# Performance work log

Hardware: AMD Instinct MI355X
Metric: run time of the kernel (lower is better)

## Reference

```python
import jax, jax.numpy as jnp
import numpy as np

N_NODES = 4096
D_FEAT = 256


def _interp_linear_2x(x):
    # Matches F.interpolate(mode='linear', scale_factor=2, align_corners=False)
    # applied along the node axis. x: [N, D] -> [2N, D]
    n = x.shape[0]
    out_i = jnp.arange(2 * n, dtype=jnp.float32)
    src = jnp.clip((out_i + 0.5) * 0.5 - 0.5, 0.0, float(n - 1))
    i0 = jnp.floor(src).astype(jnp.int32)
    i1 = jnp.minimum(i0 + 1, n - 1)
    w = (src - i0.astype(jnp.float32))[:, None]
    return x[i0] * (1.0 - w) + x[i1] * w


def _nearest_neighbor_idx(x):
    # argmin over pairwise Euclidean distances with diagonal excluded.
    # Squared distances give the same argmin as torch.cdist.
    sq = jnp.sum(x * x, axis=1)
    d2 = sq[:, None] + sq[None, :] - 2.0 * (x @ x.T)  # [2N, 2N]
    m = x.shape[0]
    d2 = jnp.where(jnp.eye(m, dtype=bool), jnp.inf, d2)
    return jnp.argmin(d2, axis=1)


def setup_inputs() -> dict:
    key = jax.random.key(0)
    k1, k2, k3, k4 = jax.random.split(key, 4)
    x = jax.random.normal(k1, (N_NODES, D_FEAT), dtype=jnp.float32)
    adj = jax.random.uniform(k2, (N_NODES, N_NODES), dtype=jnp.float32)
    # Xavier-uniform-ish init for the two GCN weights
    lim = float(np.sqrt(6.0 / (D_FEAT + D_FEAT)))
    W1 = jax.random.uniform(k3, (D_FEAT, D_FEAT), jnp.float32, -lim, lim)
    W2 = jax.random.uniform(k4, (D_FEAT, D_FEAT), jnp.float32, -lim, lim)
    return {"x": x, "adj": adj, "W1": W1, "W2": W2}


def reference(x, adj, W1, W2):
    # conv1: adj @ (x @ W1)
    h = adj @ (x @ W1)                      # [N, D]
    x2 = _interp_linear_2x(h)               # [2N, D]
    # nearest-neighbor one-hot adjacency, then conv2.
    # one_hot(nn_idx) @ support == support[nn_idx] (exact same math)
    nn_idx = _nearest_neighbor_idx(x2)      # [2N]
    support = x2 @ W2                       # [2N, D]
    return support[nn_idx]                  # [2N, D]
```

## Files before the change

kernel.cpp:

```cpp
#include <hip/hip_runtime.h>
#include <hip/hip_bf16.h>
#include <cstdint>

typedef __attribute__((ext_vector_type(8))) __bf16 bf16x8;
typedef __attribute__((ext_vector_type(4))) float f32x4;

static __device__ __forceinline__ unsigned short f2bf(float f) {
  return __builtin_bit_cast(unsigned short, (__bf16)f);
}
static __device__ __forceinline__ unsigned pack2(float a, float b) {
  return (unsigned)f2bf(a) | ((unsigned)f2bf(b) << 16);
}
#define GLDS(src, dst) __builtin_amdgcn_global_load_lds( \
    (const __attribute__((address_space(1))) void*)(src), \
    (__attribute__((address_space(3))) void*)(dst), 16, 0, 0)


__global__ void transpose_w_kernel(const float* __restrict__ W1, const float* __restrict__ W2,
                                   unsigned short* __restrict__ W1t, unsigned short* __restrict__ W2t) {
  int i = blockIdx.x * 256 + threadIdx.x;
  int k = i >> 8, n = i & 255;
  W1t[n * 256 + k] = f2bf(W1[k * 256 + n]);
  W2t[n * 256 + k] = f2bf(W2[k * 256 + n]);
}

__global__ void upsample_kernel(const unsigned short* __restrict__ hs,
                                unsigned short* __restrict__ x2b, float* __restrict__ sq) {
  int row = blockIdx.x * 4 + (threadIdx.x >> 6);
  int c = (threadIdx.x & 63) * 4;
  float s = (row + 0.5f) * 0.5f - 0.5f;
  s = fminf(fmaxf(s, 0.0f), 4095.0f);
  float fl = floorf(s);
  int i0 = (int)fl;
  int i1 = min((int)fl + 1, 4095);
  float w = s - fl;
  float v0[4] = {0.f, 0.f, 0.f, 0.f}, v1[4] = {0.f, 0.f, 0.f, 0.f};
  #pragma unroll
  for (int k = 0; k < 8; ++k) {
    ushort4 u0 = *(const ushort4*)&hs[(size_t)k * 4096 * 256 + i0 * 256 + c];
    ushort4 u1 = *(const ushort4*)&hs[(size_t)k * 4096 * 256 + i1 * 256 + c];
    v0[0] += __builtin_bit_cast(float, (unsigned)u0.x << 16);
    v0[1] += __builtin_bit_cast(float, (unsigned)u0.y << 16);
    v0[2] += __builtin_bit_cast(float, (unsigned)u0.z << 16);
    v0[3] += __builtin_bit_cast(float, (unsigned)u0.w << 16);
    v1[0] += __builtin_bit_cast(float, (unsigned)u1.x << 16);
    v1[1] += __builtin_bit_cast(float, (unsigned)u1.y << 16);
    v1[2] += __builtin_bit_cast(float, (unsigned)u1.z << 16);
    v1[3] += __builtin_bit_cast(float, (unsigned)u1.w << 16);
  }
  float p = 0.f;
  ushort4 st;
  unsigned short* sp = (unsigned short*)&st;
  #pragma unroll
  for (int e = 0; e < 4; ++e) {
    float v = v0[e] * (1.0f - w) + v1[e] * w;
    sp[e] = f2bf(v);
    p += v * v;
  }
  *(ushort4*)&x2b[(size_t)row * 256 + c] = st;
  #pragma unroll
  for (int m = 32; m > 0; m >>= 1) p += __shfl_down(p, m, 64);
  if ((threadIdx.x & 63) == 0) sq[row] = p;
}

__launch_bounds__(512)
__global__ void adj_gemm_kernel(const float* __restrict__ adjp,
                                const unsigned short* __restrict__ Ttp,
                                unsigned short* __restrict__ hs) {
  constexpr int NT = 8;
  __shared__ alignas(16) unsigned short As[256 * 64];
  __shared__ alignas(16) unsigned short Bs[256 * 64];

  const int tid = threadIdx.x;
  const int wid = tid >> 6;
  const int lane = tid & 63;
  const int g = lane >> 4, lr = lane & 15;
  const int wr = wid >> 2;
  const int wc = wid & 3;
  const int m0 = blockIdx.x * 256;
  const int kbase = blockIdx.y * 512;
  unsigned short* outp = hs + (size_t)blockIdx.y * 4096 * 256;

  const int srow = tid >> 3;
  const int scp = tid & 7;
  const int ssc = scp ^ (srow & 7);
  const float* aB[4];
  const unsigned short* bB[4];
  #pragma unroll
  for (int it = 0; it < 4; ++it) {
    aB[it] = adjp + (size_t)(m0 + it * 64 + srow) * 4096 + kbase + ssc * 8;
    bB[it] = Ttp + (size_t)(it * 64 + srow) * 4096 + kbase + ssc * 8;
  }

  f32x4 acc[8][4];
  const f32x4 fzero = {0.f, 0.f, 0.f, 0.f};
  #pragma unroll
  for (int i = 0; i < 8; ++i)
    #pragma unroll
    for (int j = 0; j < 4; ++j) acc[i][j] = fzero;

  #pragma unroll
  for (int t = 0; t < NT; ++t) {
    #pragma unroll
    for (int it = 0; it < 4; ++it)
      GLDS(bB[it] + t * 64, Bs + (size_t)(it * 512 + wid * 64) * 8);
    #pragma unroll
    for (int it = 0; it < 4; ++it) {
      const float* src = aB[it] + t * 64;
      float4 f0 = *(const float4*)src;
      float4 f1 = *(const float4*)(src + 4);
      uint4 pk = { pack2(f0.x, f0.y), pack2(f0.z, f0.w),
                   pack2(f1.x, f1.y), pack2(f1.z, f1.w) };
      *(uint4*)&As[(it * 64 + srow) * 64 + scp * 8] = pk;
    }
    __syncthreads();
    #pragma unroll
    for (int kk = 0; kk < 2; ++kk) {
      const int ch = (kk * 4 + g) ^ (lr & 7);
      bf16x8 b[4];
      #pragma unroll
      for (int j = 0; j < 4; ++j)
        b[j] = *(const bf16x8*)&Bs[(wc * 64 + j * 16 + lr) * 64 + ch * 8];
      #pragma unroll
      for (int i = 0; i < 8; ++i) {
        bf16x8 a = *(const bf16x8*)&As[(wr * 128 + i * 16 + lr) * 64 + ch * 8];
        #pragma unroll
        for (int j = 0; j < 4; ++j)
          acc[i][j] = __builtin_amdgcn_mfma_f32_16x16x32_bf16(a, b[j], acc[i][j], 0, 0, 0);
      }
    }
    __syncthreads();
  }

  #pragma unroll
  for (int i = 0; i < 8; ++i) {
    int mrow = m0 + wr * 128 + i * 16 + g * 4;
    #pragma unroll
    for (int j = 0; j < 4; ++j) {
      int col = wc * 64 + j * 16 + lr;
      #pragma unroll
      for (int r = 0; r < 4; ++r)
        outp[(size_t)(mrow + r) * 256 + col] = f2bf(acc[i][j][r]);
    }
  }
}

__launch_bounds__(256, 3)
__global__ void gram_kernel(const unsigned short* __restrict__ X,
                            const float* __restrict__ sq,
                            unsigned* __restrict__ pv) {
  __shared__ alignas(16) unsigned short As[128 * 64];
  __shared__ alignas(16) unsigned short Bs[128 * 64];
  __shared__ unsigned mrgr[2][128];
  __shared__ unsigned mrgc[2][128];

  const int tid = threadIdx.x;
  const int wid = tid >> 6;
  const int lane = tid & 63;
  const int g = lane >> 4, lr = lane & 15;
  const int wr = wid >> 1, wc = wid & 1;

  int t0 = blockIdx.x;
  int t = (t0 & 7) * 260 + (t0 >> 3);
  int bi = (int)((sqrtf(8.0f * (float)t + 1.0f) - 1.0f) * 0.5f);
  while ((bi + 1) * (bi + 2) / 2 <= t) ++bi;
  while (bi * (bi + 1) / 2 > t) --bi;
  const int bx = bi;
  const int by = t - bi * (bi + 1) / 2;
  const int m0 = bx * 128;
  const int n0 = by * 128;
  const bool diag = (bx == by);

  const int srow = tid >> 3;
  const int ssc = (tid & 7) ^ (srow & 7);
  const unsigned short* aBase = X + (size_t)(m0 + srow) * 256 + ssc * 8;
  const unsigned short* bBase = X + (size_t)(n0 + srow) * 256 + ssc * 8;
  unsigned short* const aDst = As + (size_t)(tid >> 6) * 512;
  unsigned short* const bDst = Bs + (size_t)(tid >> 6) * 512;
  const unsigned short* const Bsrc = diag ? As : Bs;

  f32x4 acc[4][4];
  const f32x4 fzero = {0.f, 0.f, 0.f, 0.f};
  #pragma unroll
  for (int i = 0; i < 4; ++i)
    #pragma unroll
    for (int j = 0; j < 4; ++j) acc[i][j] = fzero;

  #pragma unroll
  for (int ks = 0; ks < 4; ++ks) {
    #pragma unroll
    for (int it = 0; it < 4; ++it)
      GLDS(aBase + it * 8192 + ks * 64, aDst + it * 2048);
    if (!diag) {
      #pragma unroll
      for (int it = 0; it < 4; ++it)
        GLDS(bBase + it * 8192 + ks * 64, bDst + it * 2048);
    }
    __syncthreads();
    #pragma unroll
    for (int kk = 0; kk < 2; ++kk) {
      const int ch = (kk * 4 + g) ^ (lr & 7);
      bf16x8 b[4];
      #pragma unroll
      for (int j = 0; j < 4; ++j)
        b[j] = *(const bf16x8*)&Bsrc[(wc * 64 + j * 16 + lr) * 64 + ch * 8];
      #pragma unroll
      for (int i = 0; i < 4; ++i) {
        bf16x8 a = *(const bf16x8*)&As[(wr * 64 + i * 16 + lr) * 64 + ch * 8];
        #pragma unroll
        for (int j = 0; j < 4; ++j)
          acc[i][j] = __builtin_amdgcn_mfma_f32_16x16x32_bf16(a, b[j], acc[i][j], 0, 0, 0);
      }
    }
    __syncthreads();
  }

  int jcol[4];
  float sqj[4];
  unsigned ckey[4];
  #pragma unroll
  for (int j = 0; j < 4; ++j) {
    jcol[j] = n0 + wc * 64 + j * 16 + lr;
    sqj[j] = sq[jcol[j]];
    ckey[j] = 0xFFFFFFFFu;
  }
  #pragma unroll
  for (int i = 0; i < 4; ++i) {
    #pragma unroll
    for (int r = 0; r < 4; ++r) {
      const int lrow = wr * 64 + i * 16 + g * 4 + r;
      const int irow = m0 + lrow;
      const float sqi = sq[irow];
      unsigned rk = 0xFFFFFFFFu;
      #pragma unroll
      for (int j = 0; j < 4; ++j) {
        float v = fmaf(-2.0f, acc[i][j][r], sqi + sqj[j]);
        unsigned bits = __float_as_uint(v) & 0xFFFFE000u;
        unsigned krow = bits | (unsigned)jcol[j];
        if (diag && jcol[j] == irow) krow = 0xFFFFFFFFu;
        rk = min(rk, krow);
        if (!diag) ckey[j] = min(ckey[j], bits | (unsigned)irow);
      }
      #pragma unroll
      for (int m = 1; m < 16; m <<= 1)
        rk = min(rk, (unsigned)__shfl_xor((int)rk, m, 64));
      if (lr == 0) mrgr[wc][lrow] = rk;
    }
  }
  if (!diag) {
    #pragma unroll
    for (int j = 0; j < 4; ++j) {
      ckey[j] = min(ckey[j], (unsigned)__shfl_xor((int)ckey[j], 16, 64));
      ckey[j] = min(ckey[j], (unsigned)__shfl_xor((int)ckey[j], 32, 64));
      if (g == 0) mrgc[wr][wc * 64 + j * 16 + lr] = ckey[j];
    }
  }
  __syncthreads();
  if (tid < 128) {
    pv[(size_t)by * 8192 + m0 + tid] = min(mrgr[0][tid], mrgr[1][tid]);
  } else if (!diag) {
    int c = tid - 128;
    pv[(size_t)(64 + bx) * 8192 + n0 + c] = min(mrgc[0][c], mrgc[1][c]);
  }
}

template <int BM, int BN, int WAVES_M, int KT, int EPI, bool AF32, bool GATHER>
__launch_bounds__(256)
__global__ void gemm_nt_kernel(const void* __restrict__ Ap, int lda,
                               const unsigned short* __restrict__ Bp, int ldb,
                               int M, int N,
                               float* __restrict__ Cf,
                               unsigned short* __restrict__ Cb,
                               const unsigned* __restrict__ pv) {
  constexpr int BK = 64;
  constexpr int NT = KT / BK;
  constexpr int WAVES_N = 4 / WAVES_M;
  constexpr int WM = BM / WAVES_M;
  constexpr int WN = BN / WAVES_N;
  constexpr int FM = WM / 16;
  constexpr int FN = WN / 16;
  constexpr int ASLOT = BM * 8;
  constexpr int AITER = (ASLOT + 255) / 256;
  constexpr int BITER = (BN * 8) / 256;

  __shared__ alignas(16) unsigned short As[BM * BK];
  __shared__ alignas(16) unsigned short Bs[BN * BK];
  __shared__ unsigned redp[GATHER ? 4 * 64 : 1];
  __shared__ unsigned pckl[GATHER ? 64 : 1];

  const int tid = threadIdx.x;
  const int wid = tid >> 6;
  const int lane = tid & 63;
  const int g = lane >> 4;
  const int lr = lane & 15;
  const int wr = wid / WAVES_N;
  const int wc = wid % WAVES_N;
  const int m0 = blockIdx.x * BM;
  const int n0 = blockIdx.y * BN;

  if constexpr (GATHER) {
    static_assert(!GATHER || BM == 64, "inline reduce assumes BM==64");
    const int row = tid & 63;
    const int part = tid >> 6;
    const int cr = m0 >> 7;
    unsigned best = 0xFFFFFFFFu;
    #pragma unroll
    for (int s8 = 0; s8 < 16; ++s8) {
      int s = part * 16 + s8;
      int slot = s + (s > cr ? 64 : 0);
      best = min(best, pv[(size_t)slot * 8192 + m0 + row]);
    }
    redp[part * 64 + row] = best;
    __syncthreads();
    if (tid < 64)
      pckl[tid] = min(min(redp[tid], redp[64 + tid]),
                      min(redp[128 + tid], redp[192 + tid])) & 0x1FFFu;
    __syncthreads();
  }

  const int srow = tid >> 3;
  const int ssc = (tid & 7) ^ (srow & 7);
  const float* aBF[AITER];
  const unsigned short* aBH[AITER];
  #pragma unroll
  for (int it = 0; it < AITER; ++it) {
    int r = m0 + srow + it * 32;
    if constexpr (AF32) {
      aBF[it] = (const float*)Ap + (size_t)r * (size_t)lda + ssc * 8;
    } else {
      int sr = GATHER ? (int)pckl[srow + it * 32] : r;
      aBH[it] = (const unsigned short*)Ap + (size_t)sr * (size_t)lda + ssc * 8;
    }
  }
  const unsigned short* bBase = Bp + (size_t)(n0 + srow) * (size_t)ldb + ssc * 8;
  unsigned short* const sDst = As + (size_t)wid * 512;
  unsigned short* const bDst = Bs + (size_t)wid * 512;

  f32x4 acc[FM][FN];
  const f32x4 fzero = {0.f, 0.f, 0.f, 0.f};
  #pragma unroll
  for (int i = 0; i < FM; ++i)
    #pragma unroll
    for (int j = 0; j < FN; ++j) acc[i][j] = fzero;

  #pragma unroll
  for (int t = 0; t < NT; ++t) {
    #pragma unroll
    for (int it = 0; it < BITER; ++it)
      GLDS(bBase + (size_t)it * 32 * ldb + t * 64, bDst + it * 2048);
    if constexpr (AF32) {
      #pragma unroll
      for (int it = 0; it < AITER; ++it) {
        if (ASLOT % 256 == 0 || it * 256 + tid < ASLOT) {
          const float* src = aBF[it] + t * 64;
          float4 f0 = *(const float4*)src;
          float4 f1 = *(const float4*)(src + 4);
          uint4 pk = { pack2(f0.x, f0.y), pack2(f0.z, f0.w),
                       pack2(f1.x, f1.y), pack2(f1.z, f1.w) };
          *(uint4*)&As[(it * 32 + srow) * BK + (tid & 7) * 8] = pk;
        }
      }
    } else {
      #pragma unroll
      for (int it = 0; it < AITER; ++it)
        GLDS(aBH[it] + t * 64, sDst + it * 2048);
    }
    __syncthreads();
    #pragma unroll
    for (int kk = 0; kk < 2; ++kk) {
      const int ch = (kk * 4 + g) ^ (lr & 7);
      bf16x8 a[FM], b[FN];
      #pragma unroll
      for (int i = 0; i < FM; ++i)
        a[i] = *(const bf16x8*)&As[(wr * WM + i * 16 + lr) * BK + ch * 8];
      #pragma unroll
      for (int j = 0; j < FN; ++j)
        b[j] = *(const bf16x8*)&Bs[(wc * WN + j * 16 + lr) * BK + ch * 8];
      #pragma unroll
      for (int i = 0; i < FM; ++i)
        #pragma unroll
        for (int j = 0; j < FN; ++j)
          acc[i][j] = __builtin_amdgcn_mfma_f32_16x16x32_bf16(a[i], b[j], acc[i][j], 0, 0, 0);
    }
    __syncthreads();
  }

  const int rowb = wr * WM;
  const int colb = wc * WN;
  if constexpr (EPI == 0) {
    #pragma unroll
    for (int i = 0; i < FM; ++i) {
      int mrow = m0 + rowb + i * 16 + g * 4;
      #pragma unroll
      for (int j = 0; j < FN; ++j) {
        int col = n0 + colb + j * 16 + lr;
        #pragma unroll
        for (int r = 0; r < 4; ++r)
          Cf[(size_t)(mrow + r) * N + col] = acc[i][j][r];
      }
    }
  } else {
    #pragma unroll
    for (int i = 0; i < FM; ++i) {
      int mrow = m0 + rowb + i * 16 + g * 4;
      #pragma unroll
      for (int j = 0; j < FN; ++j) {
        int col = n0 + colb + j * 16 + lr;
        ushort4 st;
        st.x = f2bf(acc[i][j][0]);
        st.y = f2bf(acc[i][j][1]);
        st.z = f2bf(acc[i][j][2]);
        st.w = f2bf(acc[i][j][3]);
        *(ushort4*)&Cb[(size_t)col * M + mrow] = st;
      }
    }
  }
}


extern "C" void kernel_launch(void* const* d_in, const int* in_sizes, int n_in,
                              void* d_out, int out_size, void* d_ws, size_t ws_size,
                              hipStream_t stream) {
  (void)in_sizes; (void)n_in; (void)out_size; (void)ws_size;
  const float* x   = (const float*)d_in[0];
  const float* adj = (const float*)d_in[1];
  const float* W1  = (const float*)d_in[2];
  const float* W2  = (const float*)d_in[3];
  float* out = (float*)d_out;

  char* p = (char*)d_ws;
  unsigned short* Tt  = (unsigned short*)p;  p += 4096 * 256 * 2;
  char* R             = p;                   p += 16 * 1024 * 1024;
  unsigned short* x2b = (unsigned short*)p;  p += 8192 * 256 * 2;
  float* sqv          = (float*)p;           p += 8192 * 4;
  unsigned short* W1t = (unsigned short*)p;  p += 256 * 256 * 2;
  unsigned short* W2t = (unsigned short*)p;  p += 256 * 256 * 2;

  unsigned short* hs = (unsigned short*)R;
  unsigned* pv       = (unsigned*)R;

  transpose_w_kernel<<<256, 256, 0, stream>>>(W1, W2, W1t, W2t);

  gemm_nt_kernel<64, 64, 4, 256, 1, true, false><<<dim3(64, 4), 256, 0, stream>>>(
      x, 256, W1t, 256, 4096, 256, nullptr, Tt, nullptr);

  adj_gemm_kernel<<<dim3(16, 8), 512, 0, stream>>>(adj, Tt, hs);

  upsample_kernel<<<2048, 256, 0, stream>>>(hs, x2b, sqv);

  gram_kernel<<<2080, 256, 0, stream>>>(x2b, sqv, pv);

  gemm_nt_kernel<64, 64, 4, 256, 0, false, true><<<dim3(128, 4), 256, 0, stream>>>(
      x2b, 256, W2t, 256, 8192, 256, out, nullptr, pv);
}
```

Baseline: 98.81 us.

## Load adj fp32 tiles asynchronously into LDS and convert to bf16 at fragment read

The adjacency GEMM now stages fp32 adj tiles straight into shared memory with global_load_lds and converts them to bf16 only when building MFMA fragments, so the synchronous register round-trip for the A operand goes away. The block tile shrinks from 256x256 with 512 threads to 64x256 with 256 threads, giving 512 blocks instead of 128 for better CU coverage, at the cost of reloading the B tile more often. The gram kernel also drops its blockIdx swizzle and uses a linear triangular tile order instead.

```diff
diff --git a/kernel.cpp b/kernel.cpp
--- a/kernel.cpp
+++ b/kernel.cpp
@@ -63,67 +63,70 @@
   if ((threadIdx.x & 63) == 0) sq[row] = p;
 }
 
-__launch_bounds__(512)
+__launch_bounds__(256)
 __global__ void adj_gemm_kernel(const float* __restrict__ adjp,
                                 const unsigned short* __restrict__ Ttp,
                                 unsigned short* __restrict__ hs) {
   constexpr int NT = 8;
-  __shared__ alignas(16) unsigned short As[256 * 64];
+  __shared__ alignas(16) float Asf[64 * 64];
   __shared__ alignas(16) unsigned short Bs[256 * 64];
 
   const int tid = threadIdx.x;
   const int wid = tid >> 6;
   const int lane = tid & 63;
   const int g = lane >> 4, lr = lane & 15;
-  const int wr = wid >> 2;
-  const int wc = wid & 3;
-  const int m0 = blockIdx.x * 256;
+  const int m0 = blockIdx.x * 64;
   const int kbase = blockIdx.y * 512;
   unsigned short* outp = hs + (size_t)blockIdx.y * 4096 * 256;
 
-  const int srow = tid >> 3;
-  const int scp = tid & 7;
-  const int ssc = scp ^ (srow & 7);
+  const int arow = tid >> 4;
+  const int acp = tid & 15;
+  const int asc = acp ^ (arow & 7);
   const float* aB[4];
-  const unsigned short* bB[4];
-  #pragma unroll
-  for (int it = 0; it < 4; ++it) {
-    aB[it] = adjp + (size_t)(m0 + it * 64 + srow) * 4096 + kbase + ssc * 8;
-    bB[it] = Ttp + (size_t)(it * 64 + srow) * 4096 + kbase + ssc * 8;
-  }
-
-  f32x4 acc[8][4];
+  #pragma unroll
+  for (int it = 0; it < 4; ++it)
+    aB[it] = adjp + (size_t)(m0 + it * 16 + arow) * 4096 + kbase + asc * 4;
+  float* const aDst = Asf + (size_t)wid * 256;
+
+  const int brow = tid >> 3;
+  const int bsc = (tid & 7) ^ (brow & 7);
+  const unsigned short* bBase = Ttp + (size_t)brow * 4096 + kbase + bsc * 8;
+  unsigned short* const bDst = Bs + (size_t)wid * 512;
+
+  f32x4 acc[4][4];
   const f32x4 fzero = {0.f, 0.f, 0.f, 0.f};
   #pragma unroll
-  for (int i = 0; i < 8; ++i)
+  for (int i = 0; i < 4; ++i)
     #pragma unroll
     for (int j = 0; j < 4; ++j) acc[i][j] = fzero;
 
+  const float4* Asf4 = (const float4*)Asf;
+
   #pragma unroll
   for (int t = 0; t < NT; ++t) {
     #pragma unroll
+    for (int it = 0; it < 8; ++it)
+      GLDS(bBase + (size_t)it * 32 * 4096 + t * 64, bDst + it * 2048);
+    #pragma unroll
     for (int it = 0; it < 4; ++it)
-      GLDS(bB[it] + t * 64, Bs + (size_t)(it * 512 + wid * 64) * 8);
-    #pragma unroll
-    for (int it = 0; it < 4; ++it) {
-      const float* src = aB[it] + t * 64;
-      float4 f0 = *(const float4*)src;
-      float4 f1 = *(const float4*)(src + 4);
-      uint4 pk = { pack2(f0.x, f0.y), pack2(f0.z, f0.w),
-                   pack2(f1.x, f1.y), pack2(f1.z, f1.w) };
-      *(uint4*)&As[(it * 64 + srow) * 64 + scp * 8] = pk;
-    }
+      GLDS(aB[it] + t * 64, aDst + it * 1024);
     __syncthreads();
     #pragma unroll
     for (int kk = 0; kk < 2; ++kk) {
-      const int ch = (kk * 4 + g) ^ (lr & 7);
+      const int chb = (kk * 4 + g) ^ (lr & 7);
       bf16x8 b[4];
       #pragma unroll
       for (int j = 0; j < 4; ++j)
-        b[j] = *(const bf16x8*)&Bs[(wc * 64 + j * 16 + lr) * 64 + ch * 8];
-      #pragma unroll
-      for (int i = 0; i < 8; ++i) {
-        bf16x8 a = *(const bf16x8*)&As[(wr * 128 + i * 16 + lr) * 64 + ch * 8];
+        b[j] = *(const bf16x8*)&Bs[(wid * 64 + j * 16 + lr) * 64 + chb * 8];
+      const int c0 = kk * 8 + g * 2;
+      #pragma unroll
+      for (int i = 0; i < 4; ++i) {
+        const int row = i * 16 + lr;
+        float4 f0 = Asf4[row * 16 + (c0 ^ (lr & 7))];
+        float4 f1 = Asf4[row * 16 + ((c0 + 1) ^ (lr & 7))];
+        uint4 pk = { pack2(f0.x, f0.y), pack2(f0.z, f0.w),
+                     pack2(f1.x, f1.y), pack2(f1.z, f1.w) };
+        bf16x8 a = __builtin_bit_cast(bf16x8, pk);
         #pragma unroll
         for (int j = 0; j < 4; ++j)
           acc[i][j] = __builtin_amdgcn_mfma_f32_16x16x32_bf16(a, b[j], acc[i][j], 0, 0, 0);
@@ -133,11 +136,11 @@
   }
 
   #pragma unroll
-  for (int i = 0; i < 8; ++i) {
-    int mrow = m0 + wr * 128 + i * 16 + g * 4;
+  for (int i = 0; i < 4; ++i) {
+    int mrow = m0 + i * 16 + g * 4;
     #pragma unroll
     for (int j = 0; j < 4; ++j) {
-      int col = wc * 64 + j * 16 + lr;
+      int col = wid * 64 + j * 16 + lr;
       #pragma unroll
       for (int r = 0; r < 4; ++r)
         outp[(size_t)(mrow + r) * 256 + col] = f2bf(acc[i][j][r]);
@@ -160,8 +163,7 @@
   const int g = lane >> 4, lr = lane & 15;
   const int wr = wid >> 1, wc = wid & 1;
 
-  int t0 = blockIdx.x;
-  int t = (t0 & 7) * 260 + (t0 >> 3);
+  int t = blockIdx.x;
   int bi = (int)((sqrtf(8.0f * (float)t + 1.0f) - 1.0f) * 0.5f);
   while ((bi + 1) * (bi + 2) / 2 <= t) ++bi;
   while (bi * (bi + 1) / 2 > t) --bi;
@@ -444,7 +446,7 @@
   gemm_nt_kernel<64, 64, 4, 256, 1, true, false><<<dim3(64, 4), 256, 0, stream>>>(
       x, 256, W1t, 256, 4096, 256, nullptr, Tt, nullptr);
 
-  adj_gemm_kernel<<<dim3(16, 8), 512, 0, stream>>>(adj, Tt, hs);
+  adj_gemm_kernel<<<dim3(64, 8), 256, 0, stream>>>(adj, Tt, hs);
 
   upsample_kernel<<<2048, 256, 0, stream>>>(hs, x2b, sqv);
 
```

Measured after the change: 87.63 us. -11.3%, faster.
